# Kernel optimization log

Hardware: AMD Instinct MI355X
Metric: run time of the kernel (lower is better)

## Reference

```python
import jax, jax.numpy as jnp
import numpy as np

N = 100000      # nodes
E = 1600000     # edges
R = 4           # relations
F = 128         # node feature dim
EMB = 128       # embedding size
HID = 256       # hidden size
B = 1024        # number of (nest, food) queries


def setup_inputs() -> dict:
    key = jax.random.key(0)
    ks = jax.random.split(key, 12)
    s1 = 1.0 / np.sqrt(F)
    s2 = 1.0 / np.sqrt(EMB)
    sf = 1.0 / np.sqrt(2 * EMB)
    return {
        "x": jax.random.normal(ks[0], (N, F), jnp.float32),
        "edge_index": jax.random.randint(ks[1], (2, E), 0, N),
        "edge_type": jax.random.randint(ks[2], (E,), 0, R),
        "nest_idx": jax.random.randint(ks[3], (B,), 0, N),
        "food_idx": jax.random.randint(ks[4], (B,), 0, N),
        "W_rel1": jax.random.normal(ks[5], (R, F, EMB), jnp.float32) * s1,
        "W_root1": jax.random.normal(ks[6], (F, EMB), jnp.float32) * s1,
        "b1": jnp.zeros((EMB,), jnp.float32),
        "W_rel2": jax.random.normal(ks[7], (R, EMB, EMB), jnp.float32) * s2,
        "W_root2": jax.random.normal(ks[8], (EMB, EMB), jnp.float32) * s2,
        "b2": jnp.zeros((EMB,), jnp.float32),
        "W_fc": jax.random.normal(ks[9], (2 * EMB, HID), jnp.float32) * sf,
        "b_fc": jnp.zeros((HID,), jnp.float32),
    }


def rgcn_conv(x, src, dst, etype, W_rel, W_root, b):
    # Per-relation transform of all nodes: [N, R, O]
    h = jnp.einsum('nf,rfo->nro', x, W_rel)
    msgs = h[src, etype]                      # [E, O] gather per edge
    # Mean aggregation per (dst, relation), PyG RGCNConv default
    key = dst * R + etype                     # [E]
    deg = jax.ops.segment_sum(jnp.ones((E,), x.dtype), key, num_segments=N * R)
    norm = 1.0 / jnp.maximum(deg, 1.0)
    out = jax.ops.segment_sum(msgs * norm[key][:, None], dst, num_segments=N)
    return out + x @ W_root + b


def reference(x, edge_index, edge_type, nest_idx, food_idx,
              W_rel1, W_root1, b1, W_rel2, W_root2, b2, W_fc, b_fc):
    src, dst = edge_index[0], edge_index[1]
    h = jax.nn.relu(rgcn_conv(x, src, dst, edge_type, W_rel1, W_root1, b1))
    h = rgcn_conv(h, src, dst, edge_type, W_rel2, W_root2, b2)
    combined = jnp.concatenate([h[nest_idx], h[food_idx]], axis=-1)  # [B, 2*EMB]
    return jax.nn.relu(combined @ W_fc + b_fc)                        # [B, HID]
```

## Files before the change

### kernel.cpp

```cpp
#include <hip/hip_runtime.h>
#include <stdint.h>

#define NN 100000
#define NE 1600000
#define NR 4
#define NK (NN * NR)
#define FD 128
#define KA 512
#define KT 640
#define NQ 1024
#define HIDN 256

#define NB 391
#define BSH 8
#define CAPB 8192
#define EPB 4096
#define NBLK1 ((NE + EPB - 1) / EPB)
#define MPAD 100096

using u16 = unsigned short;
using u32 = unsigned int;
typedef __attribute__((ext_vector_type(8))) __bf16 bf16x8;
typedef __attribute__((ext_vector_type(4))) float f32x4;

__device__ __forceinline__ u16 f2b(float f) {
    u32 u = __builtin_bit_cast(u32, f);
    u32 r = u + 0x7FFFu + ((u >> 16) & 1u);
    return (u16)(r >> 16);
}
__device__ __forceinline__ float b2f_lo(u32 v) { return __builtin_bit_cast(float, v << 16); }
__device__ __forceinline__ float b2f_hi(u32 v) { return __builtin_bit_cast(float, v & 0xFFFF0000u); }
__device__ __forceinline__ u32 pack2(float a, float b) {
    return (u32)f2b(a) | ((u32)f2b(b) << 16);
}
__device__ __forceinline__ void gload_lds16(const void* g, void* l) {
    __builtin_amdgcn_global_load_lds((const __attribute__((address_space(1))) u32*)g,
                                     (__attribute__((address_space(3))) u32*)l, 16, 0, 0);
}

__global__ __launch_bounds__(256) void bucket_scatter(const int* __restrict__ ei,
                                                      const int* __restrict__ et,
                                                      int* __restrict__ bcnt,
                                                      u32* __restrict__ bpack) {
    __shared__ int hist[NB];
    __shared__ int base[NB];
    int t = threadIdx.x;
    for (int i = t; i < NB; i += 256) hist[i] = 0;
    __syncthreads();
    int e0 = blockIdx.x * EPB;
    int rank[16];
    u32 pk[16];
    int bk[16];
#pragma unroll
    for (int j = 0; j < 16; ++j) {
        int e = e0 + j * 256 + t;
        bk[j] = -1;
        if (e < NE) {
            int src = __builtin_nontemporal_load(ei + e);
            int dst = __builtin_nontemporal_load(ei + NE + e);
            int r   = __builtin_nontemporal_load(et + e);
            bk[j] = dst >> BSH;
            pk[j] = (u32)src | ((u32)r << 17) | ((u32)(dst & 255) << 19);
            rank[j] = atomicAdd(&hist[bk[j]], 1);
        }
    }
    __syncthreads();
    for (int i = t; i < NB; i += 256) {
        int h = hist[i];
        base[i] = h ? atomicAdd(&bcnt[i], h) : 0;
    }
    __syncthreads();
#pragma unroll
    for (int j = 0; j < 16; ++j)
        if (bk[j] >= 0) bpack[(size_t)bk[j] * CAPB + base[bk[j]] + rank[j]] = pk[j];
}

__global__ __launch_bounds__(256) void key_scatter(const int* __restrict__ bcnt,
                                                   const u32* __restrict__ bpack,
                                                   int* __restrict__ offs6,
                                                   int* __restrict__ spack) {
    __shared__ int hist[1024];
    __shared__ int sm[256];
    int b = blockIdx.x, t = threadIdx.x;
    int cnt = bcnt[b];
    const u32* seg = bpack + (size_t)b * CAPB;
#pragma unroll
    for (int j = 0; j < 4; ++j) hist[t + j * 256] = 0;
    __syncthreads();
    for (int i = t; i < cnt; i += 256) atomicAdd(&hist[seg[i] >> 17], 1);
    __syncthreads();
    int t4 = t * 4;
    int h0 = hist[t4], h1 = hist[t4 + 1], h2 = hist[t4 + 2], h3 = hist[t4 + 3];
    int s = h0 + h1 + h2 + h3;
    int sp = (s + 7) & ~7;
    sm[t] = sp;
    __syncthreads();
    for (int o2 = 1; o2 < 256; o2 <<= 1) {
        int n = (t >= o2) ? sm[t - o2] : 0;
        __syncthreads();
        sm[t] += n;
        __syncthreads();
    }
    int bas = b * CAPB + sm[t] - sp;
    int e0 = bas, e1 = e0 + h0, e2 = e1 + h1, e3 = e2 + h2, e4 = e3 + h3, eL = bas + sp;
    int node = (b << 8) + t;
    if (node < NN) {
        int* o = offs6 + (size_t)node * 6;
        o[0] = e0; o[1] = e1; o[2] = e2; o[3] = e3; o[4] = e4; o[5] = eL;
    }
    hist[t4] = e0; hist[t4 + 1] = e1; hist[t4 + 2] = e2; hist[t4 + 3] = e3;
    for (int i = e4; i < eL; ++i) spack[i] = NN;
    __syncthreads();
    for (int i = t; i < cnt; i += 256) {
        u32 pk = seg[i];
        int pos = atomicAdd(&hist[pk >> 17], 1);
        spack[pos] = (int)(pk & 0x1FFFFu);
    }
}

__global__ __launch_bounds__(256) void cvt_bf16(const float* __restrict__ in,
                                                u16* __restrict__ outp, int n) {
    int i = blockIdx.x * 256 + threadIdx.x;
    int idx = i * 4;
    if (idx >= n) return;
    float4 v = *(const float4*)(in + idx);
    u32 lo = (u32)f2b(v.x) | ((u32)f2b(v.y) << 16);
    u32 hi = (u32)f2b(v.z) | ((u32)f2b(v.w) << 16);
    *(uint2*)(outp + idx) = make_uint2(lo, hi);
}

__global__ __launch_bounds__(256) void prep_B(const float* __restrict__ Wrel,
                                              const float* __restrict__ Wroot,
                                              u16* __restrict__ Bt) {
    int i = blockIdx.x * 256 + threadIdx.x;
    if (i >= FD * KT) return;
    int k = i % KT;
    int o = i / KT;
    float v = (k < 512) ? Wrel[(size_t)k * FD + o] : Wroot[(size_t)(k - 512) * FD + o];
    Bt[i] = f2b(v);
}

__global__ __launch_bounds__(256) void agg_kernel(const int* __restrict__ offs6,
                                                  const int* __restrict__ spack,
                                                  const u32* __restrict__ fp,
                                                  u16* __restrict__ Aout,
                                                  int rows,
                                                  const int* __restrict__ nest,
                                                  const int* __restrict__ food,
                                                  int qmode,
                                                  int* __restrict__ qnodes) {
    int wid = threadIdx.x >> 6, lane = threadIdx.x & 63;
    int row = blockIdx.x * 4 + wid;
    if (row >= rows) return;
    int node;
    if (qmode) node = (row < NQ) ? nest[row] : food[row - NQ];
    else node = row;
    node = __builtin_amdgcn_readfirstlane(node);
    if (qmode && lane == 0) qnodes[row] = node;

    const int* ob = offs6 + (size_t)node * 6;
    int o0 = __builtin_amdgcn_readfirstlane(ob[0]);
    int o1 = __builtin_amdgcn_readfirstlane(ob[1]);
    int o2 = __builtin_amdgcn_readfirstlane(ob[2]);
    int o3 = __builtin_amdgcn_readfirstlane(ob[3]);
    int o4 = __builtin_amdgcn_readfirstlane(ob[4]);
    int oL = __builtin_amdgcn_readfirstlane(ob[5]);

    float a00 = 0, a01 = 0, a10 = 0, a11 = 0, a20 = 0, a21 = 0, a30 = 0, a31 = 0;

    for (int e = o0; e < oL; e += 8) {
        int p[8];
        u32 v[8];
#pragma unroll
        for (int j = 0; j < 8; ++j)
            p[j] = __builtin_amdgcn_readfirstlane(spack[e + j]);
#pragma unroll
        for (int j = 0; j < 8; ++j) v[j] = fp[(size_t)p[j] * 64 + lane];
#pragma unroll
        for (int j = 0; j < 8; ++j) {
            int ij = e + j;
            float f0 = b2f_lo(v[j]);
            float f1 = b2f_hi(v[j]);
            if (ij < o1)      { a00 += f0; a01 += f1; }
            else if (ij < o2) { a10 += f0; a11 += f1; }
            else if (ij < o3) { a20 += f0; a21 += f1; }
            else              { a30 += f0; a31 += f1; }
        }
    }

    int d0 = o1 - o0, d1 = o2 - o1, d2 = o3 - o2, d3 = o4 - o3;
    float s0 = 1.0f / (float)(d0 > 1 ? d0 : 1);
    float s1 = 1.0f / (float)(d1 > 1 ? d1 : 1);
    float s2 = 1.0f / (float)(d2 > 1 ? d2 : 1);
    float s3 = 1.0f / (float)(d3 > 1 ? d3 : 1);
    u16* Ao = Aout + (size_t)row * KA + lane * 2;
    __builtin_nontemporal_store(pack2(a00 * s0, a01 * s0), (u32*)(Ao + 0));
    __builtin_nontemporal_store(pack2(a10 * s1, a11 * s1), (u32*)(Ao + 128));
    __builtin_nontemporal_store(pack2(a20 * s2, a21 * s2), (u32*)(Ao + 256));
    __builtin_nontemporal_store(pack2(a30 * s3, a31 * s3), (u32*)(Ao + 384));
}

__global__ __launch_bounds__(256) void gemm_lds3(const u16* __restrict__ A,
                                                 const u16* __restrict__ rootSrc,
                                                 const int* __restrict__ rootIdx,
                                                 const u16* __restrict__ Bt,
                                                 const float* __restrict__ bias,
                                                 void* __restrict__ Cout,
                                                 int M, int relu, int outBf16) {
    __shared__ u16 As[3][8192];
    int tid = threadIdx.x;
    int wid = tid >> 6, lane = tid & 63;
    int wm = wid >> 1, wn = wid & 1;
    int lr = lane & 15, hi = lane >> 4;
    int row0 = blockIdx.x * 128;

    f32x4 acc[4][4];
#pragma unroll
    for (int i = 0; i < 4; ++i)
#pragma unroll
        for (int j = 0; j < 4; ++j) acc[i][j] = (f32x4){0.f, 0.f, 0.f, 0.f};

    int srow = wid * 8 + (lane >> 3);
    int sg = (lane & 7) ^ ((lane >> 3) & 7);

    auto stage = [&](int t, int buf) {
#pragma unroll
        for (int i = 0; i < 4; ++i) {
            int r = i * 32 + srow;
            int gr = row0 + r;
            const u16* src;
            if (t < 8) {
                src = A + (size_t)gr * KA + t * 64 + sg * 8;
            } else {
                int idx = rootIdx ? rootIdx[gr] : gr;
                src = rootSrc + (size_t)idx * FD + (t - 8) * 64 + sg * 8;
            }
            gload_lds16(src, (char*)As[buf] + i * 4096 + wid * 1024);
        }
    };

    stage(0, 0);
    stage(1, 1);

    for (int t = 0; t < 10; ++t) {
        int cur = t % 3;
        bf16x8 bfr[2][4];
#pragma unroll
        for (int kk = 0; kk < 2; ++kk)
#pragma unroll
            for (int ni = 0; ni < 4; ++ni) {
                int col = wn * 64 + ni * 16 + lr;
                bfr[kk][ni] = *reinterpret_cast<const bf16x8*>(
                    Bt + (size_t)col * KT + t * 64 + kk * 32 + hi * 8);
            }
        bool staged = (t + 2 < 10);
        if (staged) stage(t + 2, (t + 2) % 3);
        if (staged) asm volatile("s_waitcnt vmcnt(4)" ::: "memory");
        else        asm volatile("s_waitcnt vmcnt(0)" ::: "memory");
        __builtin_amdgcn_s_barrier();
        __builtin_amdgcn_sched_barrier(0);
#pragma unroll
        for (int kk = 0; kk < 2; ++kk) {
            bf16x8 afr[4];
#pragma unroll
            for (int mi = 0; mi < 4; ++mi) {
                int r = wm * 64 + mi * 16 + lr;
                int sp = (kk * 4 + hi) ^ (r & 7);
                afr[mi] = *reinterpret_cast<const bf16x8*>((char*)As[cur] + r * 128 + sp * 16);
            }
#pragma unroll
            for (int mi = 0; mi < 4; ++mi)
#pragma unroll
                for (int ni = 0; ni < 4; ++ni)
                    acc[mi][ni] = __builtin_amdgcn_mfma_f32_16x16x32_bf16(afr[mi], bfr[kk][ni], acc[mi][ni], 0, 0, 0);
        }
        asm volatile("s_waitcnt lgkmcnt(0)" ::: "memory");
        __builtin_amdgcn_s_barrier();
    }

#pragma unroll
    for (int mi = 0; mi < 4; ++mi) {
#pragma unroll
        for (int ni = 0; ni < 4; ++ni) {
            int col = wn * 64 + ni * 16 + lr;
            float bv = bias[col];
#pragma unroll
            for (int rg = 0; rg < 4; ++rg) {
                int row = row0 + wm * 64 + mi * 16 + hi * 4 + rg;
                if (row < M) {
                    float v = acc[mi][ni][rg] + bv;
                    if (relu) v = fmaxf(v, 0.f);
                    if (outBf16) ((u16*)Cout)[(size_t)row * FD + col] = f2b(v);
                    else ((float*)Cout)[(size_t)row * FD + col] = v;
                }
            }
        }
    }
}

__global__ __launch_bounds__(256) void fc_kernel(const float* __restrict__ h2q,
                                                 const float* __restrict__ Wfc,
                                                 const float* __restrict__ bfc,
                                                 float* __restrict__ out) {
    __shared__ float comb[2 * FD];
    int q = blockIdx.x, t = threadIdx.x;
    if (t < FD) comb[t] = h2q[(size_t)q * FD + t];
    else comb[t] = h2q[(size_t)(NQ + q) * FD + (t - FD)];
    __syncthreads();
    float s = bfc[t];
#pragma unroll 4
    for (int k = 0; k < 2 * FD; ++k) s += comb[k] * Wfc[(size_t)k * HIDN + t];
    out[(size_t)q * HIDN + t] = fmaxf(s, 0.f);
}

extern "C" void kernel_launch(void* const* d_in, const int* in_sizes, int n_in,
                              void* d_out, int out_size, void* d_ws, size_t ws_size,
                              hipStream_t stream) {
    const float* x      = (const float*)d_in[0];
    const int*   ei     = (const int*)d_in[1];
    const int*   et     = (const int*)d_in[2];
    const int*   nest   = (const int*)d_in[3];
    const int*   food   = (const int*)d_in[4];
    const float* Wrel1  = (const float*)d_in[5];
    const float* Wroot1 = (const float*)d_in[6];
    const float* b1     = (const float*)d_in[7];
    const float* Wrel2  = (const float*)d_in[8];
    const float* Wroot2 = (const float*)d_in[9];
    const float* b2     = (const float*)d_in[10];
    const float* Wfc    = (const float*)d_in[11];
    const float* bfc    = (const float*)d_in[12];
    float* out = (float*)d_out;

    char* w = (char*)d_ws;
    size_t off = 0;
    auto take = [&](size_t b) {
        char* p = w + off;
        off += b;
        off = (off + 255) & ~(size_t)255;
        return p;
    };
    int* bcnt   = (int*)take((size_t)NB * 4);
    int* offs6  = (int*)take((size_t)NN * 6 * 4);
    u32* bpack  = (u32*)take((size_t)NB * CAPB * 4);
    int* spack  = (int*)take((size_t)NB * CAPB * 4);
    int* qnodes = (int*)take((size_t)2 * NQ * 4);
    u16* xh     = (u16*)take((size_t)MPAD * FD * 2);
    u16* h1     = (u16*)take((size_t)MPAD * FD * 2);
    u16* Bt1    = (u16*)take((size_t)FD * KT * 2);
    u16* Bt2    = (u16*)take((size_t)FD * KT * 2);
    u16* A1     = (u16*)take((size_t)MPAD * KA * 2);
    u16* A2     = (u16*)take((size_t)2 * NQ * KA * 2);
    float* h2q  = (float*)take((size_t)2 * NQ * FD * 4);

    hipMemsetAsync(bcnt, 0, (size_t)NB * 4, stream);
    hipMemsetAsync(xh + (size_t)NN * FD, 0, FD * 2, stream);
    hipMemsetAsync(h1 + (size_t)NN * FD, 0, FD * 2, stream);
    cvt_bf16<<<((NN * FD / 4) + 255) / 256, 256, 0, stream>>>(x, xh, NN * FD);
    prep_B<<<(FD * KT + 255) / 256, 256, 0, stream>>>(Wrel1, Wroot1, Bt1);
    prep_B<<<(FD * KT + 255) / 256, 256, 0, stream>>>(Wrel2, Wroot2, Bt2);
    bucket_scatter<<<NBLK1, 256, 0, stream>>>(ei, et, bcnt, bpack);
    key_scatter<<<NB, 256, 0, stream>>>(bcnt, bpack, offs6, spack);

    agg_kernel<<<(NN + 3) / 4, 256, 0, stream>>>(offs6, spack, (const u32*)xh, A1,
                                                 NN, nullptr, nullptr, 0, nullptr);
    gemm_lds3<<<MPAD / 128, 256, 0, stream>>>(A1, xh, nullptr, Bt1, b1,
                                              (void*)h1, NN, 1, 1);

    agg_kernel<<<(2 * NQ + 3) / 4, 256, 0, stream>>>(offs6, spack, (const u32*)h1, A2,
                                                     2 * NQ, nest, food, 1, qnodes);
    gemm_lds3<<<(2 * NQ) / 128, 256, 0, stream>>>(A2, h1, qnodes, Bt2, b2,
                                                  (void*)h2q, 2 * NQ, 0, 0);
    fc_kernel<<<NQ, 256, 0, stream>>>(h2q, Wfc, bfc, out);
}
```

Before: 259.8 us.

## Transform-then-aggregate layer 1: per-relation GEMM first, gather transformed rows

```diff
diff --git a/kernel.cpp b/kernel.cpp
--- a/kernel.cpp
+++ b/kernel.cpp
@@ -17,6 +17,7 @@
 #define EPB 4096
 #define NBLK1 ((NE + EPB - 1) / EPB)
 #define MPAD 100096
+#define NCHK (MPAD / 128)
 
 using u16 = unsigned short;
 using u32 = unsigned int;
@@ -78,7 +79,7 @@
 __global__ __launch_bounds__(256) void key_scatter(const int* __restrict__ bcnt,
                                                    const u32* __restrict__ bpack,
                                                    int* __restrict__ offs6,
-                                                   int* __restrict__ spack) {
+                                                   int* __restrict__ spackY) {
     __shared__ int hist[1024];
     __shared__ int sm[256];
     int b = blockIdx.x, t = threadIdx.x;
@@ -109,12 +110,12 @@
         o[0] = e0; o[1] = e1; o[2] = e2; o[3] = e3; o[4] = e4; o[5] = eL;
     }
     hist[t4] = e0; hist[t4 + 1] = e1; hist[t4 + 2] = e2; hist[t4 + 3] = e3;
-    for (int i = e4; i < eL; ++i) spack[i] = NN;
+    for (int i = e4; i < eL; ++i) spackY[i] = 5 * NN;
     __syncthreads();
     for (int i = t; i < cnt; i += 256) {
         u32 pk = seg[i];
         int pos = atomicAdd(&hist[pk >> 17], 1);
-        spack[pos] = (int)(pk & 0x1FFFFu);
+        spackY[pos] = (int)(pk & 0x1FFFFu) + (int)((pk >> 17) & 3u) * NN;
     }
 }
 
@@ -129,6 +130,20 @@
     *(uint2*)(outp + idx) = make_uint2(lo, hi);
 }
 
+__global__ __launch_bounds__(256) void prep_B5(const float* __restrict__ Wrel,
+                                               const float* __restrict__ Wroot,
+                                               u16* __restrict__ Bt5) {
+    int i = blockIdx.x * 256 + threadIdx.x;
+    if (i >= 5 * FD * FD) return;
+    int tb = i / (FD * FD);
+    int rem = i - tb * (FD * FD);
+    int o = rem / FD;
+    int k = rem - o * FD;
+    float v = (tb < 4) ? Wrel[(size_t)tb * FD * FD + (size_t)k * FD + o]
+                       : Wroot[(size_t)k * FD + o];
+    Bt5[i] = f2b(v);
+}
+
 __global__ __launch_bounds__(256) void prep_B(const float* __restrict__ Wrel,
                                               const float* __restrict__ Wroot,
                                               u16* __restrict__ Bt) {
@@ -140,23 +155,85 @@
     Bt[i] = f2b(v);
 }
 
-__global__ __launch_bounds__(256) void agg_kernel(const int* __restrict__ offs6,
-                                                  const int* __restrict__ spack,
-                                                  const u32* __restrict__ fp,
-                                                  u16* __restrict__ Aout,
-                                                  int rows,
-                                                  const int* __restrict__ nest,
-                                                  const int* __restrict__ food,
-                                                  int qmode,
-                                                  int* __restrict__ qnodes) {
+__global__ __launch_bounds__(256) void gemm_y(const u16* __restrict__ X,
+                                              const u16* __restrict__ Bt5,
+                                              u16* __restrict__ Y) {
+    __shared__ u16 As[2][8192];
+    int blk = blockIdx.x;
+    int rel = blk / NCHK;
+    int chunk = blk - rel * NCHK;
+    int row0 = chunk * 128;
+    int tid = threadIdx.x;
+    int wid = tid >> 6, lane = tid & 63;
+    int wm = wid >> 1, wn = wid & 1;
+    int lr = lane & 15, hi = lane >> 4;
+    const u16* Btr = Bt5 + (size_t)rel * FD * FD;
+    u16* C = Y + (size_t)rel * NN * FD;
+
+    int srow = wid * 8 + (lane >> 3);
+    int sg = (lane & 7) ^ ((lane >> 3) & 7);
+#pragma unroll
+    for (int s = 0; s < 2; ++s)
+#pragma unroll
+        for (int i = 0; i < 4; ++i) {
+            int r = i * 32 + srow;
+            int gr = row0 + r;
+            gload_lds16(X + (size_t)gr * FD + s * 64 + sg * 8,
+                        (char*)As[s] + i * 4096 + wid * 1024);
+        }
+    __syncthreads();
+
+    f32x4 acc[4][4];
+#pragma unroll
+    for (int i = 0; i < 4; ++i)
+#pragma unroll
+        for (int j = 0; j < 4; ++j) acc[i][j] = (f32x4){0.f, 0.f, 0.f, 0.f};
+
+#pragma unroll
+    for (int t = 0; t < 2; ++t) {
+#pragma unroll
+        for (int kk = 0; kk < 2; ++kk) {
+            bf16x8 bfr[4], afr[4];
+#pragma unroll
+            for (int ni = 0; ni < 4; ++ni) {
+                int col = wn * 64 + ni * 16 + lr;
+                bfr[ni] = *reinterpret_cast<const bf16x8*>(
+                    Btr + (size_t)col * FD + t * 64 + kk * 32 + hi * 8);
+            }
+#pragma unroll
+            for (int mi = 0; mi < 4; ++mi) {
+                int r = wm * 64 + mi * 16 + lr;
+                int sp = (kk * 4 + hi) ^ (r & 7);
+                afr[mi] = *reinterpret_cast<const bf16x8*>((char*)As[t] + r * 128 + sp * 16);
+            }
+#pragma unroll
+            for (int mi = 0; mi < 4; ++mi)
+#pragma unroll
+                for (int ni = 0; ni < 4; ++ni)
+                    acc[mi][ni] = __builtin_amdgcn_mfma_f32_16x16x32_bf16(afr[mi], bfr[ni], acc[mi][ni], 0, 0, 0);
+        }
+    }
+#pragma unroll
+    for (int mi = 0; mi < 4; ++mi)
+#pragma unroll
+        for (int ni = 0; ni < 4; ++ni) {
+            int col = wn * 64 + ni * 16 + lr;
+#pragma unroll
+            for (int rg = 0; rg < 4; ++rg) {
+                int row = row0 + wm * 64 + mi * 16 + hi * 4 + rg;
+                if (row < NN) C[(size_t)row * FD + col] = f2b(acc[mi][ni][rg]);
+            }
+        }
+}
+
+__global__ __launch_bounds__(256) void agg_l1(const int* __restrict__ offs6,
+                                              const int* __restrict__ spackY,
+                                              const u32* __restrict__ Y,
+                                              const float* __restrict__ bias,
+                                              u16* __restrict__ h1) {
     int wid = threadIdx.x >> 6, lane = threadIdx.x & 63;
-    int row = blockIdx.x * 4 + wid;
-    if (row >= rows) return;
-    int node;
-    if (qmode) node = (row < NQ) ? nest[row] : food[row - NQ];
-    else node = row;
-    node = __builtin_amdgcn_readfirstlane(node);
-    if (qmode && lane == 0) qnodes[row] = node;
+    int node = blockIdx.x * 4 + wid;
+    if (node >= NN) return;
 
     const int* ob = offs6 + (size_t)node * 6;
     int o0 = __builtin_amdgcn_readfirstlane(ob[0]);
@@ -173,9 +250,9 @@
         u32 v[8];
 #pragma unroll
         for (int j = 0; j < 8; ++j)
-            p[j] = __builtin_amdgcn_readfirstlane(spack[e + j]);
-#pragma unroll
-        for (int j = 0; j < 8; ++j) v[j] = fp[(size_t)p[j] * 64 + lane];
+            p[j] = __builtin_amdgcn_readfirstlane(spackY[e + j]);
+#pragma unroll
+        for (int j = 0; j < 8; ++j) v[j] = Y[(size_t)p[j] * 64 + lane];
 #pragma unroll
         for (int j = 0; j < 8; ++j) {
             int ij = e + j;
@@ -193,11 +270,56 @@
     float s1 = 1.0f / (float)(d1 > 1 ? d1 : 1);
     float s2 = 1.0f / (float)(d2 > 1 ? d2 : 1);
     float s3 = 1.0f / (float)(d3 > 1 ? d3 : 1);
+    float sum0 = a00 * s0 + a10 * s1 + a20 * s2 + a30 * s3;
+    float sum1 = a01 * s0 + a11 * s1 + a21 * s2 + a31 * s3;
+    u32 rv = Y[((size_t)4 * NN + node) * 64 + lane];
+    float2 bb = *reinterpret_cast<const float2*>(bias + lane * 2);
+    float r0 = fmaxf(sum0 + b2f_lo(rv) + bb.x, 0.f);
+    float r1 = fmaxf(sum1 + b2f_hi(rv) + bb.y, 0.f);
+    *(u32*)(h1 + (size_t)node * FD + lane * 2) = pack2(r0, r1);
+}
+
+__global__ __launch_bounds__(256) void agg_q(const int* __restrict__ offs6,
+                                             const int* __restrict__ spackY,
+                                             const u32* __restrict__ fp,
+                                             u16* __restrict__ Aout,
+                                             const int* __restrict__ nest,
+                                             const int* __restrict__ food,
+                                             int* __restrict__ qnodes) {
+    int wid = threadIdx.x >> 6, lane = threadIdx.x & 63;
+    int row = blockIdx.x * 4 + wid;
+    if (row >= 2 * NQ) return;
+    int node = (row < NQ) ? nest[row] : food[row - NQ];
+    node = __builtin_amdgcn_readfirstlane(node);
+    if (lane == 0) qnodes[row] = node;
+    const int* ob = offs6 + (size_t)node * 6;
+    int o[5];
+#pragma unroll
+    for (int i = 0; i < 5; ++i) o[i] = __builtin_amdgcn_readfirstlane(ob[i]);
     u16* Ao = Aout + (size_t)row * KA + lane * 2;
-    __builtin_nontemporal_store(pack2(a00 * s0, a01 * s0), (u32*)(Ao + 0));
-    __builtin_nontemporal_store(pack2(a10 * s1, a11 * s1), (u32*)(Ao + 128));
-    __builtin_nontemporal_store(pack2(a20 * s2, a21 * s2), (u32*)(Ao + 256));
-    __builtin_nontemporal_store(pack2(a30 * s3, a31 * s3), (u32*)(Ao + 384));
+#pragma unroll
+    for (int r = 0; r < 4; ++r) {
+        int s = o[r], t = o[r + 1], last = t - 1;
+        float a0 = 0, a1 = 0;
+        for (int e = s; e < t; e += 8) {
+            int p[8];
+            u32 v[8];
+#pragma unroll
+            for (int j = 0; j < 8; ++j) {
+                int ij = e + j;
+                int cl = ij <= last ? ij : last;
+                int pv = __builtin_amdgcn_readfirstlane(spackY[cl]) - r * NN;
+                p[j] = (ij <= last) ? pv : NN;
+            }
+#pragma unroll
+            for (int j = 0; j < 8; ++j) v[j] = fp[(size_t)p[j] * 64 + lane];
+#pragma unroll
+            for (int j = 0; j < 8; ++j) { a0 += b2f_lo(v[j]); a1 += b2f_hi(v[j]); }
+        }
+        int d = t - s;
+        float sc = 1.0f / (float)(d > 1 ? d : 1);
+        *(u32*)(Ao + r * 128) = pack2(a0 * sc, a1 * sc);
+    }
 }
 
 __global__ __launch_bounds__(256) void gemm_lds3(const u16* __restrict__ A,
@@ -205,8 +327,7 @@
                                                  const int* __restrict__ rootIdx,
                                                  const u16* __restrict__ Bt,
                                                  const float* __restrict__ bias,
-                                                 void* __restrict__ Cout,
-                                                 int M, int relu, int outBf16) {
+                                                 float* __restrict__ Cout, int M) {
     __shared__ u16 As[3][8192];
     int tid = threadIdx.x;
     int wid = tid >> 6, lane = tid & 63;
@@ -232,7 +353,7 @@
             if (t < 8) {
                 src = A + (size_t)gr * KA + t * 64 + sg * 8;
             } else {
-                int idx = rootIdx ? rootIdx[gr] : gr;
+                int idx = rootIdx[gr];
                 src = rootSrc + (size_t)idx * FD + (t - 8) * 64 + sg * 8;
             }
             gload_lds16(src, (char*)As[buf] + i * 4096 + wid * 1024);
@@ -279,7 +400,7 @@
     }
 
 #pragma unroll
-    for (int mi = 0; mi < 4; ++mi) {
+    for (int mi = 0; mi < 4; ++mi)
 #pragma unroll
         for (int ni = 0; ni < 4; ++ni) {
             int col = wn * 64 + ni * 16 + lr;
@@ -287,15 +408,9 @@
 #pragma unroll
             for (int rg = 0; rg < 4; ++rg) {
                 int row = row0 + wm * 64 + mi * 16 + hi * 4 + rg;
-                if (row < M) {
-                    float v = acc[mi][ni][rg] + bv;
-                    if (relu) v = fmaxf(v, 0.f);
-                    if (outBf16) ((u16*)Cout)[(size_t)row * FD + col] = f2b(v);
-                    else ((float*)Cout)[(size_t)row * FD + col] = v;
-                }
-            }
-        }
-    }
+                if (row < M) Cout[(size_t)row * FD + col] = acc[mi][ni][rg] + bv;
+            }
+        }
 }
 
 __global__ __launch_bounds__(256) void fc_kernel(const float* __restrict__ h2q,
@@ -342,33 +457,32 @@
     int* bcnt   = (int*)take((size_t)NB * 4);
     int* offs6  = (int*)take((size_t)NN * 6 * 4);
     u32* bpack  = (u32*)take((size_t)NB * CAPB * 4);
-    int* spack  = (int*)take((size_t)NB * CAPB * 4);
+    int* spackY = (int*)take((size_t)NB * CAPB * 4);
     int* qnodes = (int*)take((size_t)2 * NQ * 4);
     u16* xh     = (u16*)take((size_t)MPAD * FD * 2);
     u16* h1     = (u16*)take((size_t)MPAD * FD * 2);
-    u16* Bt1    = (u16*)take((size_t)FD * KT * 2);
+    u16* Bt5    = (u16*)take((size_t)5 * FD * FD * 2);
     u16* Bt2    = (u16*)take((size_t)FD * KT * 2);
-    u16* A1     = (u16*)take((size_t)MPAD * KA * 2);
+    u16* Y      = (u16*)take(((size_t)5 * NN + 1) * FD * 2);
     u16* A2     = (u16*)take((size_t)2 * NQ * KA * 2);
     float* h2q  = (float*)take((size_t)2 * NQ * FD * 4);
 
     hipMemsetAsync(bcnt, 0, (size_t)NB * 4, stream);
-    hipMemsetAsync(xh + (size_t)NN * FD, 0, FD * 2, stream);
     hipMemsetAsync(h1 + (size_t)NN * FD, 0, FD * 2, stream);
+    hipMemsetAsync(Y + (size_t)5 * NN * FD, 0, FD * 2, stream);
     cvt_bf16<<<((NN * FD / 4) + 255) / 256, 256, 0, stream>>>(x, xh, NN * FD);
-    prep_B<<<(FD * KT + 255) / 256, 256, 0, stream>>>(Wrel1, Wroot1, Bt1);
+    prep_B5<<<(5 * FD * FD + 255) / 256, 256, 0, stream>>>(Wrel1, Wroot1, Bt5);
     prep_B<<<(FD * KT + 255) / 256, 256, 0, stream>>>(Wrel2, Wroot2, Bt2);
+
+    gemm_y<<<5 * NCHK, 256, 0, stream>>>(xh, Bt5, Y);
+
     bucket_scatter<<<NBLK1, 256, 0, stream>>>(ei, et, bcnt, bpack);
-    key_scatter<<<NB, 256, 0, stream>>>(bcnt, bpack, offs6, spack);
-
-    agg_kernel<<<(NN + 3) / 4, 256, 0, stream>>>(offs6, spack, (const u32*)xh, A1,
-                                                 NN, nullptr, nullptr, 0, nullptr);
-    gemm_lds3<<<MPAD / 128, 256, 0, stream>>>(A1, xh, nullptr, Bt1, b1,
-                                              (void*)h1, NN, 1, 1);
-
-    agg_kernel<<<(2 * NQ + 3) / 4, 256, 0, stream>>>(offs6, spack, (const u32*)h1, A2,
-                                                     2 * NQ, nest, food, 1, qnodes);
-    gemm_lds3<<<(2 * NQ) / 128, 256, 0, stream>>>(A2, h1, qnodes, Bt2, b2,
-                                                  (void*)h2q, 2 * NQ, 0, 0);
+    key_scatter<<<NB, 256, 0, stream>>>(bcnt, bpack, offs6, spackY);
+
+    agg_l1<<<(NN + 3) / 4, 256, 0, stream>>>(offs6, spackY, (const u32*)Y, b1, h1);
+
+    agg_q<<<(2 * NQ + 3) / 4, 256, 0, stream>>>(offs6, spackY, (const u32*)h1, A2,
+                                                nest, food, qnodes);
+    gemm_lds3<<<(2 * NQ) / 128, 256, 0, stream>>>(A2, h1, qnodes, Bt2, b2, h2q, 2 * NQ);
     fc_kernel<<<NQ, 256, 0, stream>>>(h2q, Wfc, bfc, out);
 }
```

Result: faster. 253.0 us (-2.6%).
